# Kernel optimization log

Hardware: AMD Instinct MI355X
Metric: run time of the kernel (lower is better)

The kernel has to match this reference:

```python
import jax, jax.numpy as jnp
import numpy as np

L = 2048           # lattice side
R = 2.777          # public-goods multiplier r
GAMMA = 0.8
ETA = 0.8
K_FERMI = 0.5      # fermi temperature used in fermiUpdate


def _plus_sum(x):
    """3x3 plus-kernel conv with circular (wrap) padding == self + 4 rolled neighbors."""
    return (x
            + jnp.roll(x, 1, 0) + jnp.roll(x, -1, 0)
            + jnp.roll(x, 1, 1) + jnp.roll(x, -1, 1))


def setup_inputs() -> dict:
    key = jax.random.key(0)
    k1, k2, k3, k4, k5 = jax.random.split(key, 5)
    return {
        "type_t_minus": jax.random.randint(k1, (L, L), 0, 2, dtype=jnp.int32),
        "type_t": jax.random.randint(k2, (L, L), 0, 2, dtype=jnp.int32),
        "Q_tensor": jax.random.normal(k3, (L * L, 2, 2), dtype=jnp.float32),
        "learning_direction": jax.random.randint(k4, (L, L), 0, 4, dtype=jnp.int32),
        "learning_probabilities": jax.random.uniform(k5, (L, L), dtype=jnp.float32),
    }


def reference(type_t_minus, type_t, Q_tensor, learning_direction, learning_probabilities):
    N = L * L
    # ---- calculation_value: per-cell payoff from the 5 overlapping PGG games ----
    c = (type_t == 1).astype(jnp.float32)   # cooperator mask
    d = (type_t == 0).astype(jnp.float32)   # defector mask
    coop_num = _plus_sum(c)                  # cooperators in own 5-cell group
    base = coop_num * (R / 5.0)
    profit = _plus_sum(base - 1.0) * c + _plus_sum(base) * d   # [L, L]

    # ---- updateQMatrix: Q[C, A, B] <- (1-eta)*Q[C,A,B] + eta*(profit + gamma*max_b Q[C,B,b]) ----
    A = type_t_minus.reshape(-1)             # previous action, [N]
    B = type_t.reshape(-1)                   # current action,  [N]
    Qb = jnp.take_along_axis(Q_tensor, B[:, None, None], axis=1)[:, 0, :]  # Q[C, B, :] -> [N, 2]
    max_values = Qb.max(axis=1)              # [N]
    flatQ = Q_tensor.reshape(N, 4)
    idx = A * 2 + B                          # flattened (A, B) index
    old = jnp.take_along_axis(flatQ, idx[:, None], axis=1)[:, 0]
    upd = (1.0 - ETA) * old + ETA * (profit.reshape(-1) + GAMMA * max_values)
    Q_new = flatQ.at[jnp.arange(N), idx].set(upd).reshape(N, 2, 2)

    # ---- fermiUpdate: gather just-updated Q[C,A,B] (== upd), compare with 4 neighbors ----
    pm = upd.reshape(L, L)                   # fermi profit matrix

    def W(shift, axis):
        return 1.0 / (1.0 + jnp.exp((pm - jnp.roll(pm, shift, axis)) / K_FERMI))

    Ws = jnp.stack([W(1, 1), W(-1, 1), W(1, 0), W(-1, 0)])        # left,right,up,down [4,L,L]
    nb = jnp.stack([jnp.roll(type_t, 1, 1), jnp.roll(type_t, -1, 1),
                    jnp.roll(type_t, 1, 0), jnp.roll(type_t, -1, 0)])
    W_sel = jnp.take_along_axis(Ws, learning_direction[None], axis=0)[0]
    nb_sel = jnp.take_along_axis(nb, learning_direction[None], axis=0)[0]
    type_t1 = jnp.where(learning_probabilities <= W_sel, nb_sel, type_t)  # [L, L] int32

    return (Q_new, type_t1, profit)
```

## Files before the change

kernel.cpp:

```cpp
#include <hip/hip_runtime.h>


#define LSIDE 2048
#define LMASK 2047
#define LSHIFT 11
#define NCELL (LSIDE * LSIDE)

__global__ __launch_bounds__(256) void spgg_lut_init(float* __restrict__ lut) {
    int idx = blockIdx.x * 256 + threadIdx.x;
    int cn_c = idx & 7;
    int cn_u = (idx >> 3) & 7;
    int cn_d = (idx >> 6) & 7;
    int cn_l = (idx >> 9) & 7;
    int cn_r = (idx >> 12) & 7;
    int ccc  = (idx >> 15) & 1;
    const float KB = 0.5554f;
    float b_c = __fmul_rn((float)cn_c, KB);
    float b_u = __fmul_rn((float)cn_u, KB);
    float b_d = __fmul_rn((float)cn_d, KB);
    float b_l = __fmul_rn((float)cn_l, KB);
    float b_r = __fmul_rn((float)cn_r, KB);
    float s0 = __fadd_rn(__fadd_rn(__fadd_rn(__fadd_rn(b_c, b_u), b_d), b_l), b_r);
    float s1 = __fadd_rn(__fadd_rn(__fadd_rn(__fadd_rn(
                   __fsub_rn(b_c, 1.0f), __fsub_rn(b_u, 1.0f)),
                   __fsub_rn(b_d, 1.0f)), __fsub_rn(b_l, 1.0f)),
                   __fsub_rn(b_r, 1.0f));
    lut[idx] = ccc ? s1 : s0;
}

__global__ __launch_bounds__(256) void spgg_fused(
    const int* __restrict__ tmin,
    const int* __restrict__ tt,
    const float* __restrict__ Q,
    const int* __restrict__ ldir,
    const float* __restrict__ lp,
    const float* __restrict__ lut,
    float* __restrict__ Qn,
    float* __restrict__ prof,
    float* __restrict__ t1out)
{
    const int tid = threadIdx.x;
    const int l   = tid & 63;
    const int idx = blockIdx.x * 256 + tid;
    const int i   = idx >> LSHIFT;
    const int j   = idx & LMASK;
    const int j0w = j & ~63;

    float4 qr  = ((const float4*)Q)[idx];
    int    A   = tmin[idx];
    int    dir = ldir[idx];
    float  pv  = lp[idx];

    unsigned long long hm;
    {
        int hv = 0;
        int o  = l % 6;
        int hr = l / 6;
        if (l < 42) {
            int col = (j0w + ((o < 3) ? (o - 3) : (o + 61))) & LMASK;
            int row = (i + hr - 3) & LMASK;
            hv = tt[(row << LSHIFT) + col];
        }
        hm = __ballot(l < 42 && hv == 1);
    }

    unsigned int E[7];
#pragma unroll
    for (int r = 0; r < 7; ++r) {
        int row = (i + r - 3) & LMASK;
        int v = tt[(row << LSHIFT) + j0w + l];
        unsigned long long mm = __ballot(v == 1);
        unsigned int h6 = (unsigned int)((hm >> (6 * r)) & 63ull);
        unsigned long long lo = (mm << 3) | (unsigned long long)(h6 & 7u);
        unsigned long long hi = (mm >> 29) | ((unsigned long long)(h6 >> 3) << 35);
        unsigned int win = (unsigned int)(((l < 58) ? (lo >> l) : (hi >> (l - 32))) & 0x7Full);
        unsigned int x = win;
        x = (x | (x << 12)) & 0x0007000Fu;
        x = (x | (x << 6))  & 0x03030303u;
        x = (x | (x << 3))  & 0x11111111u;
        E[r] = x;
    }

    unsigned int C[5];
#pragma unroll
    for (int r = 0; r < 5; ++r) {
        unsigned int e = E[r + 1];
        C[r] = E[r] + e + E[r + 2] + (e << 4) + (e >> 4);
    }

    unsigned int cn_c = (C[2] >> 12) & 7u;
    unsigned int cn_u = (C[1] >> 12) & 7u;
    unsigned int cn_d = (C[3] >> 12) & 7u;
    unsigned int cn_l = (C[2] >> 8)  & 7u;
    unsigned int cn_r = (C[2] >> 16) & 7u;
    unsigned int mcc  = (E[3] >> 12) & 1u;
    unsigned int io   = cn_c | (cn_u << 3) | (cn_d << 6) | (cn_l << 9)
                      | (cn_r << 12) | (mcc << 15);
    float p_own = lut[io];

    int di = (dir == 3) - (dir == 2);
    int dj = (dir == 1) - (dir == 0);
    int nidx = (((i + di) & LMASK) << LSHIFT) + ((j + dj) & LMASK);
    float4 qn4 = ((const float4*)Q)[nidx];
    int    An  = tmin[nidx];

    unsigned int Ca = (di < 0) ? C[0] : ((di > 0) ? C[2] : C[1]);
    unsigned int Cb = (di < 0) ? C[1] : ((di > 0) ? C[3] : C[2]);
    unsigned int Cc = (di < 0) ? C[2] : ((di > 0) ? C[4] : C[3]);
    unsigned int Eb = (di < 0) ? E[2] : ((di > 0) ? E[4] : E[3]);
    int sh = 4 * dj + 12;
    unsigned int cnc_n = (Cb >> sh) & 7u;
    unsigned int cnu_n = (Ca >> sh) & 7u;
    unsigned int cnd_n = (Cc >> sh) & 7u;
    unsigned int cnl_n = (Cb >> (sh - 4)) & 7u;
    unsigned int cnr_n = (Cb >> (sh + 4)) & 7u;
    unsigned int mnb   = (Eb >> sh) & 1u;
    unsigned int in_   = cnc_n | (cnu_n << 3) | (cnd_n << 6) | (cnl_n << 9)
                       | (cnr_n << 12) | (mnb << 15);
    float p_nb = lut[in_];

    const float ETA       = 0.8f;
    const float ONE_M_ETA = 0.2f;
    const float GAMMA     = 0.8f;
    int B  = (int)mcc;
    int Bn = (int)mnb;

    float q0 = (B == 0) ? qr.x : qr.z;
    float q1 = (B == 0) ? qr.y : qr.w;
    float mx = fmaxf(q0, q1);
    int k = A * 2 + B;
    float old = (k == 0) ? qr.x : ((k == 1) ? qr.y : ((k == 2) ? qr.z : qr.w));
    float upd = __fadd_rn(__fmul_rn(ONE_M_ETA, old),
                          __fmul_rn(ETA, __fadd_rn(p_own, __fmul_rn(GAMMA, mx))));

    float nq0 = (Bn == 0) ? qn4.x : qn4.z;
    float nq1 = (Bn == 0) ? qn4.y : qn4.w;
    float nmx = fmaxf(nq0, nq1);
    int kn = An * 2 + Bn;
    float nold = (kn == 0) ? qn4.x : ((kn == 1) ? qn4.y : ((kn == 2) ? qn4.z : qn4.w));
    float upd_nb = __fadd_rn(__fmul_rn(ONE_M_ETA, nold),
                             __fmul_rn(ETA, __fadd_rn(p_nb, __fmul_rn(GAMMA, nmx))));

    float4 qo;
    qo.x = (k == 0) ? upd : qr.x;
    qo.y = (k == 1) ? upd : qr.y;
    qo.z = (k == 2) ? upd : qr.z;
    qo.w = (k == 3) ? upd : qr.w;
    ((float4*)Qn)[idx] = qo;
    prof[idx] = p_own;

    float e1 = __fsub_rn(upd, upd_nb);
    float e2 = __fmul_rn(e1, 2.0f);
    float ex = (float)exp((double)e2);
    float W  = __fdiv_rn(1.0f, __fadd_rn(1.0f, ex));
    int sel = (pv <= W) ? Bn : B;
    t1out[idx] = (float)sel;
}

extern "C" void kernel_launch(void* const* d_in, const int* in_sizes, int n_in,
                              void* d_out, int out_size, void* d_ws, size_t ws_size,
                              hipStream_t stream) {
    const int*   type_t_minus = (const int*)d_in[0];
    const int*   type_t       = (const int*)d_in[1];
    const float* Q_tensor     = (const float*)d_in[2];
    const int*   ldir         = (const int*)d_in[3];
    const float* lprob        = (const float*)d_in[4];

    float* out   = (float*)d_out;
    float* Qn    = out;
    float* t1out = out + (size_t)4 * NCELL;
    float* prof  = out + (size_t)5 * NCELL;
    float* lut   = (float*)d_ws;

    spgg_lut_init<<<256, 256, 0, stream>>>(lut);
    spgg_fused<<<NCELL / 256, 256, 0, stream>>>(type_t_minus, type_t, Q_tensor,
                                                ldir, lprob, lut,
                                                Qn, prof, t1out);
}
```

Baseline: 246.4 us.

## Process four rows per thread with shared bitmask window; compute profit inline instead of LUT

```diff
diff --git a/kernel.cpp b/kernel.cpp
--- a/kernel.cpp
+++ b/kernel.cpp
@@ -6,69 +6,44 @@
 #define LSHIFT 11
 #define NCELL (LSIDE * LSIDE)
 
-__global__ __launch_bounds__(256) void spgg_lut_init(float* __restrict__ lut) {
-    int idx = blockIdx.x * 256 + threadIdx.x;
-    int cn_c = idx & 7;
-    int cn_u = (idx >> 3) & 7;
-    int cn_d = (idx >> 6) & 7;
-    int cn_l = (idx >> 9) & 7;
-    int cn_r = (idx >> 12) & 7;
-    int ccc  = (idx >> 15) & 1;
-    const float KB = 0.5554f;
-    float b_c = __fmul_rn((float)cn_c, KB);
-    float b_u = __fmul_rn((float)cn_u, KB);
-    float b_d = __fmul_rn((float)cn_d, KB);
-    float b_l = __fmul_rn((float)cn_l, KB);
-    float b_r = __fmul_rn((float)cn_r, KB);
-    float s0 = __fadd_rn(__fadd_rn(__fadd_rn(__fadd_rn(b_c, b_u), b_d), b_l), b_r);
-    float s1 = __fadd_rn(__fadd_rn(__fadd_rn(__fadd_rn(
-                   __fsub_rn(b_c, 1.0f), __fsub_rn(b_u, 1.0f)),
-                   __fsub_rn(b_d, 1.0f)), __fsub_rn(b_l, 1.0f)),
-                   __fsub_rn(b_r, 1.0f));
-    lut[idx] = ccc ? s1 : s0;
-}
-
 __global__ __launch_bounds__(256) void spgg_fused(
     const int* __restrict__ tmin,
     const int* __restrict__ tt,
     const float* __restrict__ Q,
     const int* __restrict__ ldir,
     const float* __restrict__ lp,
-    const float* __restrict__ lut,
     float* __restrict__ Qn,
     float* __restrict__ prof,
     float* __restrict__ t1out)
 {
     const int tid = threadIdx.x;
+    const int w   = tid >> 6;
     const int l   = tid & 63;
-    const int idx = blockIdx.x * 256 + tid;
-    const int i   = idx >> LSHIFT;
-    const int j   = idx & LMASK;
-    const int j0w = j & ~63;
-
-    float4 qr  = ((const float4*)Q)[idx];
-    int    A   = tmin[idx];
-    int    dir = ldir[idx];
-    float  pv  = lp[idx];
+    const int bx  = blockIdx.x;
+    const int tile_i = bx >> 5;
+    const int tile_j = bx & 31;
+    const int r0  = (tile_i << 4) + (w << 2);
+    const int j0w = tile_j << 6;
+    const int j   = j0w + l;
 
     unsigned long long hm;
     {
         int hv = 0;
-        int o  = l % 6;
-        int hr = l / 6;
-        if (l < 42) {
+        if (l < 60) {
+            int o  = l % 6;
+            int hr = l / 6;
             int col = (j0w + ((o < 3) ? (o - 3) : (o + 61))) & LMASK;
-            int row = (i + hr - 3) & LMASK;
+            int row = (r0 + hr - 3) & LMASK;
             hv = tt[(row << LSHIFT) + col];
         }
-        hm = __ballot(l < 42 && hv == 1);
+        hm = __ballot(l < 60 && hv == 1);
     }
 
-    unsigned int E[7];
+    unsigned int E[10];
 #pragma unroll
-    for (int r = 0; r < 7; ++r) {
-        int row = (i + r - 3) & LMASK;
-        int v = tt[(row << LSHIFT) + j0w + l];
+    for (int r = 0; r < 10; ++r) {
+        int row = (r0 + r - 3) & LMASK;
+        int v = tt[(row << LSHIFT) + j];
         unsigned long long mm = __ballot(v == 1);
         unsigned int h6 = (unsigned int)((hm >> (6 * r)) & 63ull);
         unsigned long long lo = (mm << 3) | (unsigned long long)(h6 & 7u);
@@ -81,80 +56,101 @@
         E[r] = x;
     }
 
-    unsigned int C[5];
+    unsigned int C[8];
 #pragma unroll
-    for (int r = 0; r < 5; ++r) {
-        unsigned int e = E[r + 1];
-        C[r] = E[r] + e + E[r + 2] + (e << 4) + (e >> 4);
+    for (int m = 0; m < 8; ++m) {
+        unsigned int e = E[m + 1];
+        C[m] = E[m] + e + E[m + 2] + (e << 4) + (e >> 4);
     }
 
-    unsigned int cn_c = (C[2] >> 12) & 7u;
-    unsigned int cn_u = (C[1] >> 12) & 7u;
-    unsigned int cn_d = (C[3] >> 12) & 7u;
-    unsigned int cn_l = (C[2] >> 8)  & 7u;
-    unsigned int cn_r = (C[2] >> 16) & 7u;
-    unsigned int mcc  = (E[3] >> 12) & 1u;
-    unsigned int io   = cn_c | (cn_u << 3) | (cn_d << 6) | (cn_l << 9)
-                      | (cn_r << 12) | (mcc << 15);
-    float p_own = lut[io];
-
-    int di = (dir == 3) - (dir == 2);
-    int dj = (dir == 1) - (dir == 0);
-    int nidx = (((i + di) & LMASK) << LSHIFT) + ((j + dj) & LMASK);
-    float4 qn4 = ((const float4*)Q)[nidx];
-    int    An  = tmin[nidx];
-
-    unsigned int Ca = (di < 0) ? C[0] : ((di > 0) ? C[2] : C[1]);
-    unsigned int Cb = (di < 0) ? C[1] : ((di > 0) ? C[3] : C[2]);
-    unsigned int Cc = (di < 0) ? C[2] : ((di > 0) ? C[4] : C[3]);
-    unsigned int Eb = (di < 0) ? E[2] : ((di > 0) ? E[4] : E[3]);
-    int sh = 4 * dj + 12;
-    unsigned int cnc_n = (Cb >> sh) & 7u;
-    unsigned int cnu_n = (Ca >> sh) & 7u;
-    unsigned int cnd_n = (Cc >> sh) & 7u;
-    unsigned int cnl_n = (Cb >> (sh - 4)) & 7u;
-    unsigned int cnr_n = (Cb >> (sh + 4)) & 7u;
-    unsigned int mnb   = (Eb >> sh) & 1u;
-    unsigned int in_   = cnc_n | (cnu_n << 3) | (cnd_n << 6) | (cnl_n << 9)
-                       | (cnr_n << 12) | (mnb << 15);
-    float p_nb = lut[in_];
-
+    const float KB        = 0.5554f;
     const float ETA       = 0.8f;
     const float ONE_M_ETA = 0.2f;
     const float GAMMA     = 0.8f;
-    int B  = (int)mcc;
-    int Bn = (int)mnb;
 
-    float q0 = (B == 0) ? qr.x : qr.z;
-    float q1 = (B == 0) ? qr.y : qr.w;
-    float mx = fmaxf(q0, q1);
-    int k = A * 2 + B;
-    float old = (k == 0) ? qr.x : ((k == 1) ? qr.y : ((k == 2) ? qr.z : qr.w));
-    float upd = __fadd_rn(__fmul_rn(ONE_M_ETA, old),
-                          __fmul_rn(ETA, __fadd_rn(p_own, __fmul_rn(GAMMA, mx))));
+    auto profit_of = [&](unsigned int cc, unsigned int cu, unsigned int cd,
+                         unsigned int cl, unsigned int cr, unsigned int m) -> float {
+        float b_c = __fmul_rn((float)cc, KB);
+        float b_u = __fmul_rn((float)cu, KB);
+        float b_d = __fmul_rn((float)cd, KB);
+        float b_l = __fmul_rn((float)cl, KB);
+        float b_r = __fmul_rn((float)cr, KB);
+        float s0 = __fadd_rn(__fadd_rn(__fadd_rn(__fadd_rn(b_c, b_u), b_d), b_l), b_r);
+        float s1 = __fadd_rn(__fadd_rn(__fadd_rn(__fadd_rn(
+                       __fsub_rn(b_c, 1.0f), __fsub_rn(b_u, 1.0f)),
+                       __fsub_rn(b_d, 1.0f)), __fsub_rn(b_l, 1.0f)),
+                       __fsub_rn(b_r, 1.0f));
+        return m ? s1 : s0;
+    };
 
-    float nq0 = (Bn == 0) ? qn4.x : qn4.z;
-    float nq1 = (Bn == 0) ? qn4.y : qn4.w;
-    float nmx = fmaxf(nq0, nq1);
-    int kn = An * 2 + Bn;
-    float nold = (kn == 0) ? qn4.x : ((kn == 1) ? qn4.y : ((kn == 2) ? qn4.z : qn4.w));
-    float upd_nb = __fadd_rn(__fmul_rn(ONE_M_ETA, nold),
-                             __fmul_rn(ETA, __fadd_rn(p_nb, __fmul_rn(GAMMA, nmx))));
+    auto upd_of = [&](float p, float4 q4, int Ax, int Bx, int kx) -> float {
+        float q0 = (Bx == 0) ? q4.x : q4.z;
+        float q1 = (Bx == 0) ? q4.y : q4.w;
+        float mx = fmaxf(q0, q1);
+        float old = (kx == 0) ? q4.x : ((kx == 1) ? q4.y : ((kx == 2) ? q4.z : q4.w));
+        return __fadd_rn(__fmul_rn(ONE_M_ETA, old),
+                         __fmul_rn(ETA, __fadd_rn(p, __fmul_rn(GAMMA, mx))));
+    };
 
-    float4 qo;
-    qo.x = (k == 0) ? upd : qr.x;
-    qo.y = (k == 1) ? upd : qr.y;
-    qo.z = (k == 2) ? upd : qr.z;
-    qo.w = (k == 3) ? upd : qr.w;
-    ((float4*)Qn)[idx] = qo;
-    prof[idx] = p_own;
+#pragma unroll
+    for (int t = 0; t < 4; ++t) {
+        const int row = r0 + t;
+        const int idx = (row << LSHIFT) + j;
 
-    float e1 = __fsub_rn(upd, upd_nb);
-    float e2 = __fmul_rn(e1, 2.0f);
-    float ex = (float)exp((double)e2);
-    float W  = __fdiv_rn(1.0f, __fadd_rn(1.0f, ex));
-    int sel = (pv <= W) ? Bn : B;
-    t1out[idx] = (float)sel;
+        float4 qr  = ((const float4*)Q)[idx];
+        int    A   = tmin[idx];
+        int    dir = ldir[idx];
+        float  pv  = lp[idx];
+
+        int di = (dir == 3) - (dir == 2);
+        int dj = (dir == 1) - (dir == 0);
+        int nidx = (((row + di) & LMASK) << LSHIFT) + ((j + dj) & LMASK);
+        float4 qn4 = ((const float4*)Q)[nidx];
+        int    An  = tmin[nidx];
+
+        unsigned int cn_c = (C[t + 2] >> 12) & 7u;
+        unsigned int cn_u = (C[t + 1] >> 12) & 7u;
+        unsigned int cn_d = (C[t + 3] >> 12) & 7u;
+        unsigned int cn_l = (C[t + 2] >> 8)  & 7u;
+        unsigned int cn_r = (C[t + 2] >> 16) & 7u;
+        unsigned int mcc  = (E[t + 3] >> 12) & 1u;
+        float p_own = profit_of(cn_c, cn_u, cn_d, cn_l, cn_r, mcc);
+
+        unsigned int Ca = (di < 0) ? C[t]     : ((di > 0) ? C[t + 2] : C[t + 1]);
+        unsigned int Cb = (di < 0) ? C[t + 1] : ((di > 0) ? C[t + 3] : C[t + 2]);
+        unsigned int Cc = (di < 0) ? C[t + 2] : ((di > 0) ? C[t + 4] : C[t + 3]);
+        unsigned int Eb = (di < 0) ? E[t + 2] : ((di > 0) ? E[t + 4] : E[t + 3]);
+        int sh = 4 * dj + 12;
+        unsigned int cnc_n = (Cb >> sh) & 7u;
+        unsigned int cnu_n = (Ca >> sh) & 7u;
+        unsigned int cnd_n = (Cc >> sh) & 7u;
+        unsigned int cnl_n = (Cb >> (sh - 4)) & 7u;
+        unsigned int cnr_n = (Cb >> (sh + 4)) & 7u;
+        unsigned int mnb   = (Eb >> sh) & 1u;
+        float p_nb = profit_of(cnc_n, cnu_n, cnd_n, cnl_n, cnr_n, mnb);
+
+        int B  = (int)mcc;
+        int Bn = (int)mnb;
+        int k  = A * 2 + B;
+        int kn = An * 2 + Bn;
+        float upd    = upd_of(p_own, qr,  A,  B,  k);
+        float upd_nb = upd_of(p_nb,  qn4, An, Bn, kn);
+
+        float4 qo;
+        qo.x = (k == 0) ? upd : qr.x;
+        qo.y = (k == 1) ? upd : qr.y;
+        qo.z = (k == 2) ? upd : qr.z;
+        qo.w = (k == 3) ? upd : qr.w;
+        ((float4*)Qn)[idx] = qo;
+        prof[idx] = p_own;
+
+        float e1 = __fsub_rn(upd, upd_nb);
+        float e2 = __fmul_rn(e1, 2.0f);
+        float ex = (float)exp((double)e2);
+        float W  = __fdiv_rn(1.0f, __fadd_rn(1.0f, ex));
+        int sel = (pv <= W) ? Bn : B;
+        t1out[idx] = (float)sel;
+    }
 }
 
 extern "C" void kernel_launch(void* const* d_in, const int* in_sizes, int n_in,
@@ -170,10 +166,9 @@
     float* Qn    = out;
     float* t1out = out + (size_t)4 * NCELL;
     float* prof  = out + (size_t)5 * NCELL;
-    float* lut   = (float*)d_ws;
 
-    spgg_lut_init<<<256, 256, 0, stream>>>(lut);
-    spgg_fused<<<NCELL / 256, 256, 0, stream>>>(type_t_minus, type_t, Q_tensor,
-                                                ldir, lprob, lut,
-                                                Qn, prof, t1out);
+    const int threads = 256;
+    const int blocks  = NCELL / (threads * 4);
+    spgg_fused<<<blocks, threads, 0, stream>>>(type_t_minus, type_t, Q_tensor,
+                                               ldir, lprob, Qn, prof, t1out);
 }
```

Measured after the change: 224.1 us. 1.1x faster.
